# Kernel optimization log

Hardware: AMD Instinct MI355X
Metric: run time of the kernel (lower is better)

## Reference

```python
import jax, jax.numpy as jnp
import numpy as np

B, TD, TC = 64, 800, 80
ENC, H, MA, MO = 128, 400, 10, 20
OUT = MO * 6 + 1  # 121


def _lstm(x, h0, c0, Wih, Whh, bih, bhh):
    # x: (B,T,I); PyTorch gate order i,f,g,o
    xg = jnp.einsum('bti,gi->btg', x, Wih) + (bih + bhh)  # (B,T,4H)
    def step(carry, xg_t):
        h, c = carry
        g = xg_t + h @ Whh.T
        i, f, gg, o = jnp.split(g, 4, axis=-1)
        c = jax.nn.sigmoid(f) * c + jax.nn.sigmoid(i) * jnp.tanh(gg)
        h = jax.nn.sigmoid(o) * jnp.tanh(c)
        return (h, c), h
    (_, _), hs = jax.lax.scan(step, (h0, c0), xg.transpose(1, 0, 2))
    return hs.transpose(1, 0, 2)  # (B,T,H)


def setup_inputs() -> dict:
    key = jax.random.key(0)
    ks = jax.random.split(key, 16)
    s = 0.05
    rn = lambda k, sh, sc=1.0: jax.random.normal(k, sh, jnp.float32) * sc
    I1 = 3 + ENC + H
    return {
        'strokes': rn(ks[0], (B, TD, 3)),
        'context': rn(ks[1], (B, TC, ENC)),
        'context_mask': jnp.ones((B, TC), jnp.float32),
        'h_0': rn(ks[2], (3, 2 * H), s),
        'Wih0': rn(ks[3], (4 * H, 3), s), 'Whh0': rn(ks[4], (4 * H, H), s),
        'bih0': jnp.zeros((4 * H,), jnp.float32), 'bhh0': jnp.zeros((4 * H,), jnp.float32),
        'Wih1': rn(ks[5], (4 * H, I1), s), 'Whh1': rn(ks[6], (4 * H, H), s),
        'bih1': jnp.zeros((4 * H,), jnp.float32), 'bhh1': jnp.zeros((4 * H,), jnp.float32),
        'Wih2': rn(ks[7], (4 * H, I1), s), 'Whh2': rn(ks[8], (4 * H, H), s),
        'bih2': jnp.zeros((4 * H,), jnp.float32), 'bhh2': jnp.zeros((4 * H,), jnp.float32),
        'attn_W': rn(ks[9], (3 * MA, H), s), 'attn_b': jnp.zeros((3 * MA,), jnp.float32),
        'out_W': rn(ks[10], (OUT, 3 * H), s), 'out_b': jnp.zeros((OUT,), jnp.float32),
    }


def reference(strokes, context, context_mask, h_0,
              Wih0, Whh0, bih0, bhh0,
              Wih1, Whh1, bih1, bhh1,
              Wih2, Whh2, bih2, bhh2,
              attn_W, attn_b, out_W, out_b):
    bsz = strokes.shape[0]
    # initial states: h_0[l] split into (h, c)
    init = [(jnp.broadcast_to(h_0[l, :H], (bsz, H)), jnp.broadcast_to(h_0[l, H:], (bsz, H))) for l in range(3)]

    h0s = _lstm(strokes, init[0][0], init[0][1], Wih0, Whh0, bih0, bhh0)  # (B,TD,H)

    # Gaussian monotonic attention
    p = jnp.exp(h0s @ attn_W.T + attn_b)  # (B,TD,3MA)
    alpha, beta, kappa = jnp.split(p, 3, axis=-1)
    kappa = jnp.cumsum(0.2 * kappa, axis=1)  # (B,TD,MA)
    u = jnp.arange(TC, dtype=jnp.float32)  # (TC,)
    # phi: (B,TD,TC)
    diff = kappa[:, :, None, :] - u[None, None, :, None]
    phi = jnp.sum(alpha[:, :, None, :] * jnp.exp(-beta[:, :, None, :] * diff * diff), axis=-1)
    w = jnp.einsum('btu,bue->bte', phi * context_mask[:, None, :], context)  # (B,TD,ENC)

    x1 = jnp.concatenate([strokes, h0s, w], axis=2)
    h1s = _lstm(x1, init[1][0], init[1][1], Wih1, Whh1, bih1, bhh1)
    x2 = jnp.concatenate([strokes, h1s, w], axis=2)
    h2s = _lstm(x2, init[2][0], init[2][1], Wih2, Whh2, bih2, bhh2)

    outputs = jnp.concatenate([h0s, h1s, h2s], axis=-1) @ out_W.T + out_b  # (B,TD,121)
    return outputs
```

## Files before the change

### kernel.cpp

```cpp
#include <hip/hip_runtime.h>
#include <stdint.h>

typedef unsigned short u16;
typedef __attribute__((ext_vector_type(8))) short bf16x8;
typedef __attribute__((ext_vector_type(4))) float f32x4;
typedef __attribute__((ext_vector_type(4))) int   i32x4;
typedef __attribute__((ext_vector_type(4))) unsigned short u16x4;

#define DI static __device__ __forceinline__

constexpr int B_   = 64;
constexpr int TD   = 800;
constexpr int TC   = 80;
constexpr int ENC  = 128;
constexpr int H    = 400;
constexpr int OUTN = 121;

constexpr int HP   = 416;
constexpr int KT_H = 13;
constexpr int KOP  = 1216;
constexpr int NOP  = 128;
constexpr int NBL  = 25;
constexpr int NBA  = 32;
constexpr int CSTR = 32;
constexpr int FSLOT= 32;

constexpr size_t HB_B  = (size_t)(TD+1)*B_*HP*2;
constexpr size_t WBF_B = (size_t)TD*B_*ENC*2;
constexpr size_t STR_B = (size_t)TD*B_*4*4;
constexpr size_t APK_B = (size_t)NBL*4*KT_H*64*8*2;
constexpr size_t WF_B  = (size_t)NBL*4*17*64*8*2;
constexpr size_t LOC_B = (size_t)2*B_*HP*2;

constexpr size_t OFF_HB0 = 0;
constexpr size_t OFF_HB1 = OFF_HB0 + HB_B;
constexpr size_t OFF_HB2 = OFF_HB1 + HB_B;
constexpr size_t OFF_HLO = OFF_HB2 + HB_B;
constexpr size_t OFF_WBF = OFF_HLO + HB_B;
constexpr size_t OFF_STR = OFF_WBF + WBF_B;
constexpr size_t OFF_APKH= OFF_STR + STR_B;
constexpr size_t OFF_APKL= OFF_APKH + 3*APK_B;
constexpr size_t OFF_WF1 = OFF_APKL + APK_B;
constexpr size_t OFF_WF2 = OFF_WF1 + WF_B;
constexpr size_t OFF_OUW = OFF_WF2 + WF_B;
constexpr size_t OFF_BIA = OFF_OUW + (size_t)NOP*KOP*2;
constexpr size_t OFF_CNT = OFF_BIA + (size_t)3*1600*4;
constexpr size_t OFF_XCC = OFF_CNT + (size_t)4*FSLOT*CSTR*4;
constexpr size_t OFF_FLG = OFF_XCC + (size_t)3*FSLOT*CSTR*4;
constexpr size_t OFF_HL0 = OFF_FLG + (size_t)3*FSLOT*CSTR*4;
constexpr size_t OFF_LL0 = OFF_HL0 + LOC_B;
constexpr size_t OFF_HL1 = OFF_LL0 + LOC_B;
constexpr size_t OFF_HL2 = OFF_HL1 + LOC_B;
constexpr size_t WS_NEED = OFF_HL2 + LOC_B + 256;

constexpr int LDS_DUMP = 0;
constexpr int LDS_CL   = 66560;
constexpr int LDS_EX   = 70656;
constexpr int LDS_W3   = 140288;
constexpr int LDS_BIAS = 141056;
constexpr int LDS_VERD = 141312;
constexpr int LDSB     = 141568;
constexpr int ALDS_CTX = 0;
constexpr int ALDS_ATW = 81920;
constexpr int ALDS_H   = 130040;
constexpr int ALDS_PHI = 133240;
constexpr int ALDS_MSK = 133880;
constexpr int ALDS_KAP = 134520;
constexpr int ALDS_P   = 134600;
constexpr int ALDS_PPS = 134840;

DI u16 f2b(float f){ union{float f; unsigned u;} v; v.f=f; unsigned r = v.u + 0x7FFFu + ((v.u>>16)&1u); return (u16)(r>>16); }
DI float b2f(u16 h){ union{unsigned u; float f;} v; v.u=((unsigned)h)<<16; return v.f; }
DI float sigm(float x){ return 1.f/(1.f+__expf(-x)); }
DI float tanh_(float x){ float a=fabsf(x), e=__expf(-2.f*a), t=(1.f-e)/(1.f+e); return x<0.f ? -t : t; }

DI void st16(u16* p, u16 v){
  asm volatile("global_store_short %0, %1, off sc0 sc1" :: "v"(p), "v"((unsigned)v) : "memory");
}
DI void st8(u16* p, u16x4 v){
  unsigned long long x; __builtin_memcpy(&x, &v, 8);
  asm volatile("global_store_dwordx2 %0, %1, off sc0 sc1" :: "v"(p), "v"(x) : "memory");
}
DI void setflag(unsigned* p, unsigned t){
  asm volatile("global_store_dword %0, %1, off sc0 sc1" :: "v"(p), "v"(t) : "memory");
}
DI void waitflags2(const unsigned* fA, int nA, unsigned tA,
                   const unsigned* fB, int nB, unsigned tB){
  int lane = threadIdx.x & 63;
  const unsigned* p; unsigned tgt;
  if (lane < nA)            { p = fA + (size_t)lane*CSTR;        tgt = tA; }
  else if (lane < nA+nB)    { p = fB + (size_t)(lane-nA)*CSTR;   tgt = tB; }
  else                      { p = fA;                            tgt = 0;  }
  while (1) {
    unsigned v = __hip_atomic_load(p, __ATOMIC_RELAXED, __HIP_MEMORY_SCOPE_AGENT);
    if (__all(v >= tgt)) break;
    __builtin_amdgcn_s_sleep(1);
  }
  asm volatile("" ::: "memory");
}
DI void waitloc(const unsigned* f, int n, unsigned tgt){
  int lane = threadIdx.x & 63;
  const volatile unsigned* p = (const volatile unsigned*)(f + (size_t)((lane<n)?lane:0)*CSTR);
  while (1) {
    unsigned v = *p;
    if (__all(v >= tgt)) break;
    __builtin_amdgcn_s_sleep(1);
  }
  asm volatile("" ::: "memory");
}
DI bf16x8 vld8(const u16* p){
  i32x4 v = *(const volatile i32x4*)p;
  bf16x8 r; __builtin_memcpy(&r, &v, 16); return r;
}
DI int get_xcc(){
  int x; asm volatile("s_getreg_b32 %0, hwreg(HW_REG_XCC_ID)" : "=s"(x)); return x & 0xff;
}

__global__ void k_init(const float* __restrict__ h0, u16* hb0, u16* hb1, u16* hb2, u16* hlo,
                       unsigned* cnt, unsigned* xccb, unsigned* flgb,
                       u16* hl0, u16* ll0, u16* hl1, u16* hl2){
  int i = blockIdx.x*256 + threadIdx.x;
  const int nA = 3*B_*HP, nA2 = B_*HP, nB = 4*TD*B_*16, nC = 4*FSLOT, nD = 6*FSLOT;
  const int nE = 4*2*B_*HP;
  if (i < nA) {
    int l = i/(B_*HP); int rem = i - l*(B_*HP); int b = rem/HP; int k = rem - b*HP;
    u16 v = (k<H) ? f2b(h0[l*800 + k]) : (u16)0;
    (l==0?hb0:(l==1?hb1:hb2))[(size_t)b*HP + k] = v;
  } else if (i < nA+nA2) {
    int rem = i - nA; int b = rem/HP; int k = rem - b*HP;
    u16 v = 0;
    if (k < H) { float w = h0[k]; u16 hi = f2b(w); v = f2b(w - b2f(hi)); }
    hlo[(size_t)b*HP + k] = v;
  } else if (i < nA+nA2+nB) {
    int q = i - nA - nA2; int buf = q/(TD*B_*16); int r2 = q % (TD*B_*16);
    int t = r2/(B_*16) + 1; int r3 = r2 % (B_*16); int b = r3>>4; int kk = r3&15;
    u16* hb = (buf==0)?hb0:((buf==1)?hb1:((buf==2)?hb2:hlo));
    hb[((size_t)t*B_ + b)*HP + 400 + kk] = 0;
  } else if (i < nA+nA2+nB+nC) {
    int q = i - nA - nA2 - nB;
    cnt[(size_t)q*CSTR] = 0u;
  } else if (i < nA+nA2+nB+nC+nD) {
    int q = i - nA - nA2 - nB - nC;
    if (q < 3*FSLOT) xccb[(size_t)q*CSTR] = 0u;
    else             flgb[(size_t)(q-3*FSLOT)*CSTR] = 0u;
  } else if (i < nA+nA2+nB+nC+nD+nE) {
    int q = i - nA - nA2 - nB - nC - nD;
    int buf = q / (2*B_*HP); int rem = q % (2*B_*HP);
    int k = rem % HP;
    u16 v = 0;
    if (k < H) {
      if (buf == 0)      v = f2b(h0[k]);
      else if (buf == 1) { float w = h0[k]; u16 hi = f2b(w); v = f2b(w - b2f(hi)); }
      else if (buf == 2) v = f2b(h0[800 + k]);
      else               v = f2b(h0[1600 + k]);
    }
    (buf==0?hl0:(buf==1?ll0:(buf==2?hl1:hl2)))[rem] = v;
  }
}

__global__ void k_apack(const float* W0, const float* W1, const float* W2,
                        u16* apkHi, u16* apkLo){
  int i = blockIdx.x*256 + threadIdx.x;
  const int total = 3*NBL*4*KT_H*64;
  if (i >= total) return;
  int lane = i & 63; int r = i >> 6;
  int kt = r % KT_H; r /= KT_H;
  int mt = r % 4;    r /= 4;
  int j  = r % NBL;  int lv = r / NBL;
  const float* W = (lv==0)?W0:((lv==1)?W1:W2);
  int row = mt*400 + j*16 + (lane & 15);
  int kbase = kt*32 + (lane>>4)*8;
  #pragma unroll
  for (int e=0;e<8;++e){
    int k = kbase+e;
    float w = (k<H) ? W[(size_t)row*H + k] : 0.f;
    u16 hi = f2b(w);
    apkHi[(size_t)i*8 + e] = hi;
    if (lv == 0) apkLo[(size_t)i*8 + e] = f2b(w - b2f(hi));
  }
}

__global__ void k_wihpack2(const float* __restrict__ W, u16* __restrict__ dst){
  int i = blockIdx.x*256 + threadIdx.x;
  if (i >= NBL*4*17*64) return;
  int lane = i & 63; int r = i >> 6;
  int ktf = r % 17; r /= 17; int mt = r % 4; int j = r / 4;
  int row = mt*400 + j*16 + (lane & 15);
  int kbase = ktf*32 + (lane>>4)*8;
  #pragma unroll
  for (int e=0;e<8;++e){
    int k = kbase+e;
    int col;
    if (ktf < 13) col = (k < 400) ? (3 + k) : -1;
    else          col = 403 + (k - 416);
    dst[(size_t)i*8 + e] = (col >= 0) ? f2b(W[(size_t)row*531 + col]) : (u16)0;
  }
}

__global__ void k_smallpack(const float* outW,
                            const float* bi0, const float* bh0, const float* bi1, const float* bh1,
                            const float* bi2, const float* bh2,
                            u16* ouw, float* biasP){
  int i = blockIdx.x*256 + threadIdx.x;
  const int n2 = NOP*KOP, n3 = 3*1600;
  if (i < n2) {
    int n = i/KOP, k = i - n*KOP;
    ouw[i] = (n<OUTN && k<1200) ? f2b(outW[(size_t)n*1200 + k]) : (u16)0;
  } else if (i < n2+n3) {
    int q = i-n2; int l = q/1600, row = q - l*1600;
    const float* bi = (l==0)?bi0:((l==1)?bi1:bi2);
    const float* bh = (l==0)?bh0:((l==1)?bh1:bh2);
    biasP[q] = bi[row] + bh[row];
  }
}

__global__ void k_packs(const float* __restrict__ strokes, float* __restrict__ st){
  int i = blockIdx.x*256 + threadIdx.x;
  if (i >= TD*B_) return;
  int t = i / B_, b = i & 63;
  st[(size_t)i*4+0] = strokes[((size_t)b*TD + t)*3 + 0];
  st[(size_t)i*4+1] = strokes[((size_t)b*TD + t)*3 + 1];
  st[(size_t)i*4+2] = strokes[((size_t)b*TD + t)*3 + 2];
  st[(size_t)i*4+3] = 0.f;
}

template<int L, bool LOC>
DI void stage_lstm(char* smem, int j,
    const u16* __restrict__ apkHi, const u16* __restrict__ exG,
    const float* __restrict__ strokesT,
    const float* __restrict__ wihRaw, int wihStride,
    const float* __restrict__ biasL, const float* __restrict__ h0g,
    u16* __restrict__ hb_self, const u16* __restrict__ hb_prev,
    u16* __restrict__ hlo_, const u16* __restrict__ wbf,
    unsigned* __restrict__ fSelf, const unsigned* __restrict__ fDep, int nDep,
    u16* __restrict__ hloc, u16* __restrict__ lloc, unsigned* __restrict__ flgS)
{
  float* dumpS = (float*)(smem + LDS_DUMP);
  float* cL    = (float*)(smem + LDS_CL);
  u16*   exS   = (u16*)  (smem + LDS_EX);
  float* w3S   = (float*)(smem + LDS_W3);
  float* biasS = (float*)(smem + LDS_BIAS);
  const int tid = threadIdx.x, wv = tid>>6, l = tid&63;
  const int col = l&15, kg = l>>4;

  bf16x8 ahi[4][4];
  #pragma unroll
  for (int mt=0;mt<4;++mt)
    #pragma unroll
    for (int i=0;i<4;++i){
      int kt = wv + i*4;
      if (kt < KT_H) ahi[mt][i] = *(const bf16x8*)(apkHi + (size_t)j*26624 + ((size_t)(mt*KT_H + kt)*64 + l)*8);
      else { bf16x8 z = {0,0,0,0,0,0,0,0}; ahi[mt][i] = z; }
    }
  {
    const int nv = (L==0) ? 3328 : 4352;
    const size_t stride = (L==0) ? 26624 : 34816;
    const i32x4* src = (const i32x4*)(exG + (size_t)j*stride);
    i32x4* dst = (i32x4*)exS;
    for (int i = tid; i < nv; i += 256) dst[i] = src[i];
  }
  if (tid < 192) {
    int local = tid/3, c = tid - (tid/3)*3;
    int row = (local>>4)*400 + j*16 + (local&15);
    w3S[tid] = wihRaw[(size_t)row*wihStride + c];
  }
  if (tid < 64) {
    int row = (tid>>4)*400 + j*16 + (tid&15);
    biasS[tid] = biasL[row];
  }
  for (int i = tid; i < 1024; i += 256) cL[i] = h0g[L*800 + 400 + j*16 + (i>>6)];
  __syncthreads();

  for (int t = 1; t <= TD; ++t) {
    if (wv == 0) {
      if constexpr (L > 0) waitflags2(fDep, nDep, (unsigned)t, nullptr, 0, 0u);
      if constexpr (LOC)   waitloc(flgS, NBL, (unsigned)(t-1));
      else                 waitflags2(fSelf, NBL, (unsigned)(t-1), nullptr, 0, 0u);
    }
    __syncthreads();

    const u16* hbase; const u16* lbase = nullptr;
    if constexpr (LOC) {
      hbase = hloc + (size_t)((t-1)&1)*B_*HP + kg*8;
      if constexpr (L==0) lbase = lloc + (size_t)((t-1)&1)*B_*HP + kg*8;
    } else {
      hbase = hb_self + (size_t)(t-1)*B_*HP + kg*8;
      if constexpr (L==0) lbase = hlo_ + (size_t)(t-1)*B_*HP + kg*8;
    }
    bf16x8 bh[4][4], bl[4][4], pf[5][4];
    #pragma unroll
    for (int i=0;i<4;++i){
      int kt = wv + i*4;
      if (kt < KT_H) {
        #pragma unroll
        for (int nt=0;nt<4;++nt){
          if constexpr (LOC) bh[i][nt] = vld8(hbase + (size_t)(nt*16+col)*HP + kt*32);
          else               bh[i][nt] = *(const bf16x8*)(hbase + (size_t)(nt*16+col)*HP + kt*32);
          if constexpr (L==0) {
            if constexpr (LOC) bl[i][nt] = vld8(lbase + (size_t)(nt*16+col)*HP + kt*32);
            else               bl[i][nt] = *(const bf16x8*)(lbase + (size_t)(nt*16+col)*HP + kt*32);
          }
        }
      }
    }
    if constexpr (L > 0) {
      const u16* pbase = hb_prev + (size_t)t*B_*HP + kg*8;
      const u16* wbase = wbf + ((size_t)(t-1)*B_)*ENC + kg*8;
      #pragma unroll
      for (int i=0;i<5;++i){
        int ktf = wv + i*4;
        if (ktf < 17) {
          #pragma unroll
          for (int nt=0;nt<4;++nt){
            if (ktf < 13) pf[i][nt] = *(const bf16x8*)(pbase + (size_t)(nt*16+col)*HP + ktf*32);
            else          pf[i][nt] = *(const bf16x8*)(wbase + (size_t)(nt*16+col)*ENC + (ktf-13)*32);
          }
        }
      }
    }

    f32x4 acc[4][4];
    #pragma unroll
    for (int mt=0;mt<4;++mt)
      #pragma unroll
      for (int nt=0;nt<4;++nt){ f32x4 z = {0.f,0.f,0.f,0.f}; acc[mt][nt] = z; }
    #pragma unroll
    for (int i=0;i<4;++i){
      int kt = wv + i*4;
      if (kt < KT_H) {
        #pragma unroll
        for (int mt=0;mt<4;++mt){
          bf16x8 a = ahi[mt][i];
          #pragma unroll
          for (int nt=0;nt<4;++nt)
            acc[mt][nt] = __builtin_amdgcn_mfma_f32_16x16x32_bf16(a, bh[i][nt], acc[mt][nt], 0,0,0);
          if constexpr (L==0) {
            bf16x8 al = *(const bf16x8*)(exS + ((size_t)(mt*KT_H + kt)*64 + l)*8);
            #pragma unroll
            for (int nt=0;nt<4;++nt){
              acc[mt][nt] = __builtin_amdgcn_mfma_f32_16x16x32_bf16(a,  bl[i][nt], acc[mt][nt], 0,0,0);
              acc[mt][nt] = __builtin_amdgcn_mfma_f32_16x16x32_bf16(al, bh[i][nt], acc[mt][nt], 0,0,0);
            }
          }
        }
      }
    }
    if constexpr (L > 0) {
      #pragma unroll
      for (int i=0;i<5;++i){
        int ktf = wv + i*4;
        if (ktf < 17) {
          #pragma unroll
          for (int mt=0;mt<4;++mt){
            bf16x8 a = *(const bf16x8*)(exS + ((size_t)(mt*17 + ktf)*64 + l)*8);
            #pragma unroll
            for (int nt=0;nt<4;++nt)
              acc[mt][nt] = __builtin_amdgcn_mfma_f32_16x16x32_bf16(a, pf[i][nt], acc[mt][nt], 0,0,0);
          }
        }
      }
    }
    #pragma unroll
    for (int mt=0;mt<4;++mt)
      #pragma unroll
      for (int nt=0;nt<4;++nt)
        #pragma unroll
        for (int r=0;r<4;++r)
          dumpS[wv*4160 + (mt*16 + kg*4 + r)*65 + nt*16 + col] = acc[mt][nt][r];
    __syncthreads();
    {
      const int bg = tid & 63, uq = tid >> 6;
      const float* sp = strokesT + ((size_t)(t-1)*B_ + bg)*4;
      float sx = sp[0], sy = sp[1], sz = sp[2];
      u16x4 hh4, ll4;
      #pragma unroll
      for (int e=0;e<4;++e){
        int u = uq*4 + e;
        int idx = u*64 + bg;
        float gv[4];
        #pragma unroll
        for (int g=0; g<4; ++g){
          int row = g*16 + u;
          float s = dumpS[row*65 + bg] + dumpS[4160 + row*65 + bg]
                  + dumpS[8320 + row*65 + bg] + dumpS[12480 + row*65 + bg];
          s += biasS[row] + w3S[row*3+0]*sx + w3S[row*3+1]*sy + w3S[row*3+2]*sz;
          gv[g] = s;
        }
        float co = cL[idx];
        float i_ = sigm(gv[0]), f_ = sigm(gv[1]), g_ = tanh_(gv[2]), o_ = sigm(gv[3]);
        float cn = f_*co + i_*g_;
        cL[idx] = cn;
        float hv = o_*tanh_(cn);
        u16 hh = f2b(hv);
        hh4[e] = hh;
        if constexpr (L==0) ll4[e] = f2b(hv - b2f(hh));
      }
      if constexpr (LOC) {
        *(u16x4*)(hloc + ((size_t)(t&1)*B_ + bg)*HP + j*16 + uq*4) = hh4;
        if constexpr (L==0) *(u16x4*)(lloc + ((size_t)(t&1)*B_ + bg)*HP + j*16 + uq*4) = ll4;
        if constexpr (L==2) {
          *(u16x4*)(hb_self + ((size_t)t*B_ + bg)*HP + j*16 + uq*4) = hh4;
        } else {
          st8(hb_self + ((size_t)t*B_ + bg)*HP + j*16 + uq*4, hh4);
          if constexpr (L==0) st8(hlo_ + ((size_t)t*B_ + bg)*HP + j*16 + uq*4, ll4);
        }
      } else {
        st8(hb_self + ((size_t)t*B_ + bg)*HP + j*16 + uq*4, hh4);
        if constexpr (L==0) st8(hlo_ + ((size_t)t*B_ + bg)*HP + j*16 + uq*4, ll4);
      }
    }
    __syncthreads();
    if (tid == 0) {
      if constexpr (LOC) *((volatile unsigned*)(flgS + (size_t)j*CSTR)) = (unsigned)t;
      setflag(fSelf + (size_t)j*CSTR, (unsigned)t);
    }
  }
}

DI void stage_attn(char* smem, int j2,
    const float* __restrict__ ctx, const float* __restrict__ cmask,
    const float* __restrict__ attnW, const float* __restrict__ attnB,
    const u16* __restrict__ hb0, const u16* __restrict__ hlo_,
    u16* __restrict__ wbf,
    const unsigned* __restrict__ fA, unsigned* __restrict__ fB)
{
  float* ctxS = (float*)(smem + ALDS_CTX);
  float* atwS = (float*)(smem + ALDS_ATW);
  float* hS   = (float*)(smem + ALDS_H);
  float* phiS = (float*)(smem + ALDS_PHI);
  float* mskS = (float*)(smem + ALDS_MSK);
  float* kapS = (float*)(smem + ALDS_KAP);
  float* pS   = (float*)(smem + ALDS_P);
  float* ppsS = (float*)(smem + ALDS_PPS);
  const int tid = threadIdx.x;
  const int b0 = j2*2;
  for (int i = tid; i < 2*80*128; i += 256) {
    int bi = i/10240, rem = i%10240;
    ctxS[i] = ctx[(size_t)(b0+bi)*10240 + rem];
  }
  for (int i = tid; i < 30*400; i += 256) {
    int row = i/400, k = i - row*400;
    atwS[row*401 + k] = attnW[i];
  }
  for (int i = tid; i < 160; i += 256) {
    int bi = i/80, u = i - bi*80;
    mskS[i] = cmask[(b0+bi)*80 + u];
  }
  if (tid < 20) kapS[tid] = 0.f;
  float aB = (tid < 60) ? attnB[tid % 30] : 0.f;
  __syncthreads();

  for (int t = 1; t <= TD; ++t) {
    if ((tid>>6) == 0) waitflags2(fA, NBL, (unsigned)t, nullptr, 0, 0u);
    __syncthreads();
    if (tid < 200) {
      int bi = tid/100, k = (tid%100)*4;
      size_t off = ((size_t)t*B_ + (b0+bi))*HP + k;
      u16x4 hi4 = *(const u16x4*)(hb0 + off);
      u16x4 lo4 = *(const u16x4*)(hlo_ + off);
      #pragma unroll
      for (int e=0;e<4;++e) hS[bi*400 + k + e] = b2f(hi4[e]) + b2f(lo4[e]);
    }
    __syncthreads();
    if (tid < 240) {
      int bi = tid/120, r = tid - bi*120;
      int row = r>>2, seg = r&3;
      const float* ar = atwS + row*401 + seg*100;
      const float* hr = hS + bi*400 + seg*100;
      float a0=0,a1=0,a2=0,a3=0;
      #pragma unroll 4
      for (int k=0;k<100;k+=4){
        a0 += ar[k]*hr[k]; a1 += ar[k+1]*hr[k+1];
        a2 += ar[k+2]*hr[k+2]; a3 += ar[k+3]*hr[k+3];
      }
      ppsS[(bi*30+row)*4+seg] = a0+a1+a2+a3;
    }
    __syncthreads();
    if (tid < 60) {
      int bi = tid/30, row = tid - bi*30;
      const float* pp = ppsS + (bi*30+row)*4;
      pS[bi*30+row] = __expf(pp[0]+pp[1]+pp[2]+pp[3] + aB);
    }
    __syncthreads();
    if (tid < 20) {
      int bi = tid/10, m = tid - bi*10;
      kapS[tid] += 0.2f * pS[bi*30 + 20 + m];
    }
    __syncthreads();
    if (tid < 160) {
      int bi = tid/80; float u2 = (float)(tid - bi*80);
      const float* pb = pS + bi*30; const float* kb = kapS + bi*10;
      float a = 0.f;
      #pragma unroll
      for (int m=0;m<10;++m){ float d = kb[m]-u2; a += pb[m]*__expf(-pb[10+m]*d*d); }
      phiS[tid] = a * mskS[tid];
    }
    __syncthreads();
    {
      int bi = tid >> 7, e = tid & 127;
      const float* ph = phiS + bi*80;
      const float* cs = ctxS + (size_t)bi*10240 + e;
      float a = 0.f;
      for (int u = 0; u < TC; ++u) a += ph[u]*cs[u*128];
      st16(wbf + ((size_t)(t-1)*B_ + (b0+bi))*ENC + e, f2b(a));
    }
    __syncthreads();
    if (tid == 0) setflag(fB + (size_t)j2*CSTR, (unsigned)t);
  }
}

DI bool xcc_check(char* smem, int stage, int j, unsigned* xccb){
  unsigned* xs = xccb + (size_t)stage*FSLOT*CSTR;
  if (threadIdx.x == 0) setflag(xs + (size_t)j*CSTR, 0x100u | (unsigned)get_xcc());
  if ((threadIdx.x>>6) == 0) {
    waitflags2(xs, NBL, 0x100u, nullptr, 0, 0u);
    int lane = threadIdx.x & 63;
    unsigned v = __hip_atomic_load(xs + (size_t)((lane<NBL)?lane:0)*CSTR,
                                   __ATOMIC_RELAXED, __HIP_MEMORY_SCOPE_AGENT);
    unsigned r0 = __shfl(v, 0);
    int uni = __all(v == r0) ? 1 : 0;
    if (threadIdx.x == 0) *(int*)(smem + LDS_VERD) = uni;
  }
  __syncthreads();
  return (*(int*)(smem + LDS_VERD)) != 0;
}

__global__ __launch_bounds__(256,1) void k_mega(
    const u16* apkH, const u16* apkL, const u16* wf1, const u16* wf2,
    const float* strokesT, const float* Wih0, const float* Wih1, const float* Wih2,
    const float* bia, const float* h0g,
    u16* hb0, u16* hb1, u16* hb2, u16* hlo, u16* wbf,
    const float* ctx, const float* cmask, const float* attnW, const float* attnB,
    unsigned* cnt, unsigned* xccb, unsigned* flgb,
    u16* hl0, u16* ll0, u16* hl1, u16* hl2)
{
  extern __shared__ char smem[];
  unsigned* fA = cnt;
  unsigned* fB = cnt + (size_t)FSLOT*CSTR;
  unsigned* fC = cnt + (size_t)2*FSLOT*CSTR;
  unsigned* fD = cnt + (size_t)3*FSLOT*CSTR;
  int b = blockIdx.x; int colx = b & 7; int row = b >> 3;
  if (colx == 0 && row < NBL) {
    bool loc = xcc_check(smem, 0, row, xccb);
    if (loc) stage_lstm<0,true >(smem, row, apkH, apkL, strokesT, Wih0, 3, bia, h0g,
                  hb0, nullptr, hlo, nullptr, fA, nullptr, 0, hl0, ll0, flgb);
    else     stage_lstm<0,false>(smem, row, apkH, apkL, strokesT, Wih0, 3, bia, h0g,
                  hb0, nullptr, hlo, nullptr, fA, nullptr, 0, hl0, ll0, flgb);
  } else if ((colx == 1 || colx == 2) && row < 16) {
    int j2 = (colx-1)*16 + row;
    stage_attn(smem, j2, ctx, cmask, attnW, attnB, hb0, hlo, wbf, fA, fB);
  } else if (colx == 3 && row < NBL) {
    bool loc = xcc_check(smem, 1, row, xccb);
    unsigned* fg = flgb + (size_t)FSLOT*CSTR;
    if (loc) stage_lstm<1,true >(smem, row, apkH + (size_t)1*NBL*26624, wf1, strokesT, Wih1, 531,
                  bia+1600, h0g, hb1, hb0, nullptr, wbf, fC, fB, NBA, hl1, nullptr, fg);
    else     stage_lstm<1,false>(smem, row, apkH + (size_t)1*NBL*26624, wf1, strokesT, Wih1, 531,
                  bia+1600, h0g, hb1, hb0, nullptr, wbf, fC, fB, NBA, hl1, nullptr, fg);
  } else if (colx == 4 && row < NBL) {
    bool loc = xcc_check(smem, 2, row, xccb);
    unsigned* fg = flgb + (size_t)2*FSLOT*CSTR;
    if (loc) stage_lstm<2,true >(smem, row, apkH + (size_t)2*NBL*26624, wf2, strokesT, Wih2, 531,
                  bia+3200, h0g, hb2, hb1, nullptr, wbf, fD, fC, NBL, hl2, nullptr, fg);
    else     stage_lstm<2,false>(smem, row, apkH + (size_t)2*NBL*26624, wf2, strokesT, Wih2, 531,
                  bia+3200, h0g, hb2, hb1, nullptr, wbf, fD, fC, NBL, hl2, nullptr, fg);
  }
}

__global__ __launch_bounds__(256) void k_gemm_out(const u16* __restrict__ hb0, const u16* __restrict__ hb1,
                                                  const u16* __restrict__ hb2, const u16* __restrict__ ouw,
                                                  const float* __restrict__ out_b, float* __restrict__ dout){
  int wv = threadIdx.x>>6, l = threadIdx.x&63;
  int task = blockIdx.x*4 + wv;
  int ng = task & 1; int mpair = task >> 1;
  int m0 = mpair*32; int t = m0>>6; int broff = m0 & 63;
  int col = l&15, kg = l>>4;
  f32x4 acc[2][4];
  #pragma unroll
  for (int mt=0;mt<2;++mt)
    #pragma unroll
    for (int nt=0;nt<4;++nt){ f32x4 z = {0.f,0.f,0.f,0.f}; acc[mt][nt] = z; }
  for (int kt=0; kt<38; ++kt) {
    int k0 = kt*32 + kg*8;
    int reg = (k0>=800) ? 2 : ((k0>=400) ? 1 : 0);
    int koff = k0 - reg*400;
    const u16* hb = (reg==0) ? hb0 : ((reg==1) ? hb1 : hb2);
    bf16x8 afr[2];
    #pragma unroll
    for (int mt=0;mt<2;++mt)
      afr[mt] = *(const bf16x8*)(hb + ((size_t)(t+1)*B_ + broff + mt*16 + col)*HP + koff);
    #pragma unroll
    for (int nt=0;nt<4;++nt) {
      bf16x8 bfr = *(const bf16x8*)(ouw + (size_t)(ng*64 + nt*16 + col)*KOP + k0);
      #pragma unroll
      for (int mt=0;mt<2;++mt)
        acc[mt][nt] = __builtin_amdgcn_mfma_f32_16x16x32_bf16(afr[mt], bfr, acc[mt][nt], 0,0,0);
    }
  }
  #pragma unroll
  for (int mt=0;mt<2;++mt)
    #pragma unroll
    for (int nt=0;nt<4;++nt)
      #pragma unroll
      for (int r=0;r<4;++r) {
        int n = ng*64 + nt*16 + col;
        int bo = broff + mt*16 + kg*4 + r;
        if (n < OUTN) dout[((size_t)bo*TD + t)*OUTN + n] = acc[mt][nt][r] + out_b[n];
      }
}

__global__ void k_sentinel(float* o, float code){ o[threadIdx.x] = code; }

extern "C" void kernel_launch(void* const* d_in, const int* in_sizes, int n_in,
                              void* d_out, int out_size, void* d_ws, size_t ws_size,
                              hipStream_t stream) {
  const float* strokes = (const float*)d_in[0];
  const float* context = (const float*)d_in[1];
  const float* cmask   = (const float*)d_in[2];
  const float* h0      = (const float*)d_in[3];
  const float* Wih0 = (const float*)d_in[4];  const float* Whh0 = (const float*)d_in[5];
  const float* bih0 = (const float*)d_in[6];  const float* bhh0 = (const float*)d_in[7];
  const float* Wih1 = (const float*)d_in[8];  const float* Whh1 = (const float*)d_in[9];
  const float* bih1 = (const float*)d_in[10]; const float* bhh1 = (const float*)d_in[11];
  const float* Wih2 = (const float*)d_in[12]; const float* Whh2 = (const float*)d_in[13];
  const float* bih2 = (const float*)d_in[14]; const float* bhh2 = (const float*)d_in[15];
  const float* attnW = (const float*)d_in[16]; const float* attnB = (const float*)d_in[17];
  const float* outW  = (const float*)d_in[18]; const float* outB  = (const float*)d_in[19];
  float* dout = (float*)d_out;

  if (ws_size < WS_NEED) {
    float code = 1000.0f + (float)(ws_size >> 20);
    k_sentinel<<<1, 64, 0, stream>>>(dout, code);
    return;
  }

  char* ws = (char*)d_ws;
  u16* hb0 = (u16*)(ws + OFF_HB0);
  u16* hb1 = (u16*)(ws + OFF_HB1);
  u16* hb2 = (u16*)(ws + OFF_HB2);
  u16* hlo = (u16*)(ws + OFF_HLO);
  u16* wbf = (u16*)(ws + OFF_WBF);
  float* strT = (float*)(ws + OFF_STR);
  u16* apkH = (u16*)(ws + OFF_APKH);
  u16* apkL = (u16*)(ws + OFF_APKL);
  u16* wf1  = (u16*)(ws + OFF_WF1);
  u16* wf2  = (u16*)(ws + OFF_WF2);
  u16* ouw  = (u16*)(ws + OFF_OUW);
  float* bia = (float*)(ws + OFF_BIA);
  unsigned* cnt = (unsigned*)(ws + OFF_CNT);
  unsigned* xccb = (unsigned*)(ws + OFF_XCC);
  unsigned* flgb = (unsigned*)(ws + OFF_FLG);
  u16* hl0 = (u16*)(ws + OFF_HL0);
  u16* ll0 = (u16*)(ws + OFF_LL0);
  u16* hl1 = (u16*)(ws + OFF_HL1);
  u16* hl2 = (u16*)(ws + OFF_HL2);

  (void)hipFuncSetAttribute((const void*)k_mega, hipFuncAttributeMaxDynamicSharedMemorySize, LDSB);

  {
    int n = 3*B_*HP + B_*HP + 4*TD*B_*16 + 4*FSLOT + 6*FSLOT + 4*2*B_*HP;
    k_init<<<(n+255)/256, 256, 0, stream>>>(h0, hb0, hb1, hb2, hlo, cnt, xccb, flgb, hl0, ll0, hl1, hl2);
  }
  k_apack<<<(3*NBL*4*KT_H*64+255)/256, 256, 0, stream>>>(Whh0, Whh1, Whh2, apkH, apkL);
  k_wihpack2<<<(NBL*4*17*64+255)/256, 256, 0, stream>>>(Wih1, wf1);
  k_wihpack2<<<(NBL*4*17*64+255)/256, 256, 0, stream>>>(Wih2, wf2);
  {
    int n = NOP*KOP + 3*1600;
    k_smallpack<<<(n+255)/256, 256, 0, stream>>>(outW, bih0,bhh0,bih1,bhh1,bih2,bhh2, ouw, bia);
  }
  k_packs<<<(TD*B_+255)/256, 256, 0, stream>>>(strokes, strT);

  k_mega<<<256, 256, LDSB, stream>>>(apkH, apkL, wf1, wf2,
      strT, Wih0, Wih1, Wih2, bia, h0,
      hb0, hb1, hb2, hlo, wbf,
      context, cmask, attnW, attnB, cnt, xccb, flgb, hl0, ll0, hl1, hl2);

  k_gemm_out<<<3200/4, 256, 0, stream>>>(hb0, hb1, hb2, ouw, outB, dout);
}
```

Baseline: 7.493 ms.

## Stage cross-layer inputs into XCC-local double buffers before LSTM step

For layers 1 and 2 running on a single XCC, each block copies a slice of the previous layer's hidden state and the attention window into a small double-buffered local area, then all blocks meet at a local barrier flag before reading. The goal is for the per-step input reads to hit the XCC-local L2 instead of pulling remote, possibly uncached lines from the large history buffers. The cost is an extra copy, a __syncthreads and a cross-block barrier on every timestep, which adds latency to the sequential recurrence.

Result: slower. 8.728 ms (+16.5%).

```diff
diff --git a/kernel.cpp b/kernel.cpp
--- a/kernel.cpp
+++ b/kernel.cpp
@@ -31,6 +31,8 @@
 constexpr size_t APK_B = (size_t)NBL*4*KT_H*64*8*2;
 constexpr size_t WF_B  = (size_t)NBL*4*17*64*8*2;
 constexpr size_t LOC_B = (size_t)2*B_*HP*2;
+constexpr size_t PIN_B = (size_t)2*B_*HP*2;
+constexpr size_t WIN_B = (size_t)2*B_*ENC*2;
 
 constexpr size_t OFF_HB0 = 0;
 constexpr size_t OFF_HB1 = OFF_HB0 + HB_B;
@@ -47,11 +49,15 @@
 constexpr size_t OFF_CNT = OFF_BIA + (size_t)3*1600*4;
 constexpr size_t OFF_XCC = OFF_CNT + (size_t)4*FSLOT*CSTR*4;
 constexpr size_t OFF_FLG = OFF_XCC + (size_t)3*FSLOT*CSTR*4;
-constexpr size_t OFF_HL0 = OFF_FLG + (size_t)3*FSLOT*CSTR*4;
+constexpr size_t OFF_HL0 = OFF_FLG + (size_t)5*FSLOT*CSTR*4;
 constexpr size_t OFF_LL0 = OFF_HL0 + LOC_B;
 constexpr size_t OFF_HL1 = OFF_LL0 + LOC_B;
 constexpr size_t OFF_HL2 = OFF_HL1 + LOC_B;
-constexpr size_t WS_NEED = OFF_HL2 + LOC_B + 256;
+constexpr size_t OFF_PI1 = OFF_HL2 + LOC_B;
+constexpr size_t OFF_WI1 = OFF_PI1 + PIN_B;
+constexpr size_t OFF_PI2 = OFF_WI1 + WIN_B;
+constexpr size_t OFF_WI2 = OFF_PI2 + PIN_B;
+constexpr size_t WS_NEED = OFF_WI2 + WIN_B + 256;
 
 constexpr int LDS_DUMP = 0;
 constexpr int LDS_CL   = 66560;
@@ -120,7 +126,7 @@
                        unsigned* cnt, unsigned* xccb, unsigned* flgb,
                        u16* hl0, u16* ll0, u16* hl1, u16* hl2){
   int i = blockIdx.x*256 + threadIdx.x;
-  const int nA = 3*B_*HP, nA2 = B_*HP, nB = 4*TD*B_*16, nC = 4*FSLOT, nD = 6*FSLOT;
+  const int nA = 3*B_*HP, nA2 = B_*HP, nB = 4*TD*B_*16, nC = 4*FSLOT, nD = 8*FSLOT;
   const int nE = 4*2*B_*HP;
   if (i < nA) {
     int l = i/(B_*HP); int rem = i - l*(B_*HP); int b = rem/HP; int k = rem - b*HP;
@@ -233,7 +239,8 @@
     u16* __restrict__ hb_self, const u16* __restrict__ hb_prev,
     u16* __restrict__ hlo_, const u16* __restrict__ wbf,
     unsigned* __restrict__ fSelf, const unsigned* __restrict__ fDep, int nDep,
-    u16* __restrict__ hloc, u16* __restrict__ lloc, unsigned* __restrict__ flgS)
+    u16* __restrict__ hloc, u16* __restrict__ lloc, unsigned* __restrict__ flgS,
+    u16* __restrict__ pin, u16* __restrict__ win, unsigned* __restrict__ sgF)
 {
   float* dumpS = (float*)(smem + LDS_DUMP);
   float* cL    = (float*)(smem + LDS_CL);
@@ -278,6 +285,21 @@
       else                 waitflags2(fSelf, NBL, (unsigned)(t-1), nullptr, 0, 0u);
     }
     __syncthreads();
+
+    if constexpr (LOC && L > 0) {
+      int idx = j + tid*NBL;
+      if (idx < 3328) {
+        const i32x4* srcH = (const i32x4*)(hb_prev + (size_t)t*B_*HP);
+        ((i32x4*)(pin + (size_t)(t&1)*B_*HP))[idx] = srcH[idx];
+      }
+      if (idx < 1024) {
+        const i32x4* srcW = (const i32x4*)(wbf + (size_t)(t-1)*B_*ENC);
+        ((i32x4*)(win + (size_t)(t&1)*B_*ENC))[idx] = srcW[idx];
+      }
+      __syncthreads();
+      if (tid == 0) *((volatile unsigned*)(sgF + (size_t)j*CSTR)) = (unsigned)t;
+      waitloc(sgF, NBL, (unsigned)t);
+    }
 
     const u16* hbase; const u16* lbase = nullptr;
     if constexpr (LOC) {
@@ -304,16 +326,27 @@
       }
     }
     if constexpr (L > 0) {
-      const u16* pbase = hb_prev + (size_t)t*B_*HP + kg*8;
-      const u16* wbase = wbf + ((size_t)(t-1)*B_)*ENC + kg*8;
+      const u16* pbase; const u16* wbase;
+      if constexpr (LOC) {
+        pbase = pin + (size_t)(t&1)*B_*HP + kg*8;
+        wbase = win + (size_t)(t&1)*B_*ENC + kg*8;
+      } else {
+        pbase = hb_prev + (size_t)t*B_*HP + kg*8;
+        wbase = wbf + ((size_t)(t-1)*B_)*ENC + kg*8;
+      }
       #pragma unroll
       for (int i=0;i<5;++i){
         int ktf = wv + i*4;
         if (ktf < 17) {
           #pragma unroll
           for (int nt=0;nt<4;++nt){
-            if (ktf < 13) pf[i][nt] = *(const bf16x8*)(pbase + (size_t)(nt*16+col)*HP + ktf*32);
-            else          pf[i][nt] = *(const bf16x8*)(wbase + (size_t)(nt*16+col)*ENC + (ktf-13)*32);
+            if (ktf < 13) {
+              if constexpr (LOC) pf[i][nt] = vld8(pbase + (size_t)(nt*16+col)*HP + ktf*32);
+              else               pf[i][nt] = *(const bf16x8*)(pbase + (size_t)(nt*16+col)*HP + ktf*32);
+            } else {
+              if constexpr (LOC) pf[i][nt] = vld8(wbase + (size_t)(nt*16+col)*ENC + (ktf-13)*32);
+              else               pf[i][nt] = *(const bf16x8*)(wbase + (size_t)(nt*16+col)*ENC + (ktf-13)*32);
+            }
           }
         }
       }
@@ -532,7 +565,8 @@
     u16* hb0, u16* hb1, u16* hb2, u16* hlo, u16* wbf,
     const float* ctx, const float* cmask, const float* attnW, const float* attnB,
     unsigned* cnt, unsigned* xccb, unsigned* flgb,
-    u16* hl0, u16* ll0, u16* hl1, u16* hl2)
+    u16* hl0, u16* ll0, u16* hl1, u16* hl2,
+    u16* pi1, u16* wi1, u16* pi2, u16* wi2)
 {
   extern __shared__ char smem[];
   unsigned* fA = cnt;
@@ -543,26 +577,34 @@
   if (colx == 0 && row < NBL) {
     bool loc = xcc_check(smem, 0, row, xccb);
     if (loc) stage_lstm<0,true >(smem, row, apkH, apkL, strokesT, Wih0, 3, bia, h0g,
-                  hb0, nullptr, hlo, nullptr, fA, nullptr, 0, hl0, ll0, flgb);
+                  hb0, nullptr, hlo, nullptr, fA, nullptr, 0, hl0, ll0, flgb,
+                  nullptr, nullptr, nullptr);
     else     stage_lstm<0,false>(smem, row, apkH, apkL, strokesT, Wih0, 3, bia, h0g,
-                  hb0, nullptr, hlo, nullptr, fA, nullptr, 0, hl0, ll0, flgb);
+                  hb0, nullptr, hlo, nullptr, fA, nullptr, 0, hl0, ll0, flgb,
+                  nullptr, nullptr, nullptr);
   } else if ((colx == 1 || colx == 2) && row < 16) {
     int j2 = (colx-1)*16 + row;
     stage_attn(smem, j2, ctx, cmask, attnW, attnB, hb0, hlo, wbf, fA, fB);
   } else if (colx == 3 && row < NBL) {
     bool loc = xcc_check(smem, 1, row, xccb);
     unsigned* fg = flgb + (size_t)FSLOT*CSTR;
+    unsigned* sg = flgb + (size_t)3*FSLOT*CSTR;
     if (loc) stage_lstm<1,true >(smem, row, apkH + (size_t)1*NBL*26624, wf1, strokesT, Wih1, 531,
-                  bia+1600, h0g, hb1, hb0, nullptr, wbf, fC, fB, NBA, hl1, nullptr, fg);
+                  bia+1600, h0g, hb1, hb0, nullptr, wbf, fC, fB, NBA, hl1, nullptr, fg,
+                  pi1, wi1, sg);
     else     stage_lstm<1,false>(smem, row, apkH + (size_t)1*NBL*26624, wf1, strokesT, Wih1, 531,
-                  bia+1600, h0g, hb1, hb0, nullptr, wbf, fC, fB, NBA, hl1, nullptr, fg);
+                  bia+1600, h0g, hb1, hb0, nullptr, wbf, fC, fB, NBA, hl1, nullptr, fg,
+                  pi1, wi1, sg);
   } else if (colx == 4 && row < NBL) {
     bool loc = xcc_check(smem, 2, row, xccb);
     unsigned* fg = flgb + (size_t)2*FSLOT*CSTR;
+    unsigned* sg = flgb + (size_t)4*FSLOT*CSTR;
     if (loc) stage_lstm<2,true >(smem, row, apkH + (size_t)2*NBL*26624, wf2, strokesT, Wih2, 531,
-                  bia+3200, h0g, hb2, hb1, nullptr, wbf, fD, fC, NBL, hl2, nullptr, fg);
+                  bia+3200, h0g, hb2, hb1, nullptr, wbf, fD, fC, NBL, hl2, nullptr, fg,
+                  pi2, wi2, sg);
     else     stage_lstm<2,false>(smem, row, apkH + (size_t)2*NBL*26624, wf2, strokesT, Wih2, 531,
-                  bia+3200, h0g, hb2, hb1, nullptr, wbf, fD, fC, NBL, hl2, nullptr, fg);
+                  bia+3200, h0g, hb2, hb1, nullptr, wbf, fD, fC, NBL, hl2, nullptr, fg,
+                  pi2, wi2, sg);
   }
 }
 
@@ -653,11 +695,15 @@
   u16* ll0 = (u16*)(ws + OFF_LL0);
   u16* hl1 = (u16*)(ws + OFF_HL1);
   u16* hl2 = (u16*)(ws + OFF_HL2);
+  u16* pi1 = (u16*)(ws + OFF_PI1);
+  u16* wi1 = (u16*)(ws + OFF_WI1);
+  u16* pi2 = (u16*)(ws + OFF_PI2);
+  u16* wi2 = (u16*)(ws + OFF_WI2);
 
   (void)hipFuncSetAttribute((const void*)k_mega, hipFuncAttributeMaxDynamicSharedMemorySize, LDSB);
 
   {
-    int n = 3*B_*HP + B_*HP + 4*TD*B_*16 + 4*FSLOT + 6*FSLOT + 4*2*B_*HP;
+    int n = 3*B_*HP + B_*HP + 4*TD*B_*16 + 4*FSLOT + 8*FSLOT + 4*2*B_*HP;
     k_init<<<(n+255)/256, 256, 0, stream>>>(h0, hb0, hb1, hb2, hlo, cnt, xccb, flgb, hl0, ll0, hl1, hl2);
   }
   k_apack<<<(3*NBL*4*KT_H*64+255)/256, 256, 0, stream>>>(Whh0, Whh1, Whh2, apkH, apkL);
@@ -672,7 +718,8 @@
   k_mega<<<256, 256, LDSB, stream>>>(apkH, apkL, wf1, wf2,
       strT, Wih0, Wih1, Wih2, bia, h0,
       hb0, hb1, hb2, hlo, wbf,
-      context, cmask, attnW, attnB, cnt, xccb, flgb, hl0, ll0, hl1, hl2);
+      context, cmask, attnW, attnB, cnt, xccb, flgb, hl0, ll0, hl1, hl2,
+      pi1, wi1, pi2, wi2);
 
   k_gemm_out<<<3200/4, 256, 0, stream>>>(hb0, hb1, hb2, ouw, outB, dout);
 }
```
